# Optimization experiments

Hardware: AMD Instinct MI355X
Metric: run time of the kernel (lower is better)

The kernel has to match this reference:

```python
import jax, jax.numpy as jnp
import numpy as np

BS, NE, NN, CIN, H, D = 8, 4800, 4981, 3, 128, 6
EPG = 19200
NEDGE = BS * EPG
N = BS * NE

PARAM_NAMES = [
    'enc_cw1','enc_cb1','enc_cw2','enc_cb2','enc_cw3','enc_clng','enc_clnb',
    'enc_ew1','enc_eb1','enc_ew2','enc_eb2','enc_ew3','enc_elng','enc_elnb',
    'p_ew1','p_eb1','p_ew2','p_eb2','p_ew3','p_elng','p_elnb',
    'p_nw1','p_nb1','p_nw2','p_nb2','p_nw3','p_nlng','p_nlnb',
    'dec_uw1','dec_ub1','dec_uw2','dec_ub2','dec_uw3','dec_ulng','dec_ulnb',
    'dec_cw1','dec_cb1','dec_cw2','dec_cb2','dec_cw3']


def setup_inputs():
    key = jax.random.key(0)
    ks = iter(jax.random.split(key, 64))
    def nrm(shape, s=0.1):
        return jax.random.normal(next(ks), shape, jnp.float32) * s
    inp = {}
    inp['x'] = jax.random.normal(next(ks), (BS * NN, CIN), jnp.float32)
    inp['elem_conn'] = jax.random.randint(next(ks), (NE, 4), 0, NN)
    inp['edge_index'] = jax.random.randint(next(ks), (2, NEDGE), 0, N)
    inp['enc_cw1'] = nrm((CIN, 4, 1)); inp['enc_cb1'] = nrm((CIN, 1), 0.01)
    inp['enc_cw2'] = nrm((CIN, 1, 1)); inp['enc_cb2'] = nrm((CIN, 1), 0.01)
    inp['enc_cw3'] = nrm((CIN, 1, 1))
    inp['enc_clng'] = jnp.ones((CIN, 1)); inp['enc_clnb'] = jnp.zeros((CIN, 1))
    inp['enc_ew1'] = nrm((CIN, H)); inp['enc_eb1'] = nrm((H,), 0.01)
    inp['enc_ew2'] = nrm((H, H)); inp['enc_eb2'] = nrm((H,), 0.01)
    inp['enc_ew3'] = nrm((H, H))
    inp['enc_elng'] = jnp.ones((H,)); inp['enc_elnb'] = jnp.zeros((H,))
    inp['p_ew1'] = nrm((D, 2 * H, H)); inp['p_eb1'] = nrm((D, H), 0.01)
    inp['p_ew2'] = nrm((D, H, H)); inp['p_eb2'] = nrm((D, H), 0.01)
    inp['p_ew3'] = nrm((D, H, H))
    inp['p_elng'] = jnp.ones((D, H)); inp['p_elnb'] = jnp.zeros((D, H))
    inp['p_nw1'] = nrm((D, 2 * H, H)); inp['p_nb1'] = nrm((D, H), 0.01)
    inp['p_nw2'] = nrm((D, H, H)); inp['p_nb2'] = nrm((D, H), 0.01)
    inp['p_nw3'] = nrm((D, H, H))
    inp['p_nlng'] = jnp.ones((D, H)); inp['p_nlnb'] = jnp.zeros((D, H))
    inp['dec_uw1'] = nrm((H, 1, 4)); inp['dec_ub1'] = nrm((H, 4), 0.01)
    inp['dec_uw2'] = nrm((H, 4, 4)); inp['dec_ub2'] = nrm((H, 4), 0.01)
    inp['dec_uw3'] = nrm((H, 4, 4))
    inp['dec_ulng'] = jnp.ones((H, 4)); inp['dec_ulnb'] = jnp.zeros((H, 4))
    inp['dec_cw1'] = nrm((H, CIN)); inp['dec_cb1'] = nrm((CIN,), 0.01)
    inp['dec_cw2'] = nrm((CIN, CIN)); inp['dec_cb2'] = nrm((CIN,), 0.01)
    inp['dec_cw3'] = nrm((CIN, CIN))
    return inp


def lrelu(x):
    return jnp.where(x >= 0, x, 0.2 * x)


def ln(x, g, b, axis=-1):
    m = jnp.mean(x, axis=axis, keepdims=True)
    v = jnp.var(x, axis=axis, keepdims=True)
    return (x - m) / jnp.sqrt(v + 1e-5) * g + b


def mlp(x, w1, b1, w2, b2, w3):
    h = lrelu(x @ w1 + b1)
    h = lrelu(h @ w2 + b2)
    return h @ w3


def _forward(fl, elem_conn, edge_index):
    x = fl[0]
    P = dict(zip(PARAM_NAMES, fl[1:]))
    # ---- Encoder: MeshCNN gather (4 mesh nodes per element) + per-channel MLP 4->1 ----
    xg = x.reshape(BS, NN, CIN)[:, elem_conn]                  # (BS, NE, 4, CIN)
    h = lrelu(jnp.einsum('beic,cio->beoc', xg, P['enc_cw1']) + P['enc_cb1'].T[None, None])
    h = lrelu(jnp.einsum('beic,cio->beoc', h, P['enc_cw2']) + P['enc_cb2'].T[None, None])
    h = jnp.einsum('beic,cio->beoc', h, P['enc_cw3'])
    h = ln(h, P['enc_clng'].T[None, None], P['enc_clnb'].T[None, None], axis=2)  # LayerNorm(1)
    h = h[:, :, 0, :].reshape(N, CIN)
    h = ln(mlp(h, P['enc_ew1'], P['enc_eb1'], P['enc_ew2'], P['enc_eb2'], P['enc_ew3']),
           P['enc_elng'], P['enc_elnb'])                       # (N, H)
    # ---- Processor: D GraphNet blocks, edge MLP + scatter-add + node MLP ----
    src, dest = edge_index[0], edge_index[1]
    stacked = (P['p_ew1'], P['p_eb1'], P['p_ew2'], P['p_eb2'], P['p_ew3'], P['p_elng'], P['p_elnb'],
               P['p_nw1'], P['p_nb1'], P['p_nw2'], P['p_nb2'], P['p_nw3'], P['p_nlng'], P['p_nlnb'])
    def step(hc, p):
        ew1, eb1, ew2, eb2, ew3, eg, ebv, nw1, nb1, nw2, nb2, nw3, ng, nbv = p
        msg = jnp.concatenate([hc[dest], hc[src]], axis=-1)    # (NEDGE, 2H)
        m = ln(mlp(msg, ew1, eb1, ew2, eb2, ew3), eg, ebv)
        aggr = jax.ops.segment_sum(m, dest, num_segments=N)
        hn = ln(mlp(jnp.concatenate([hc, aggr], axis=-1), nw1, nb1, nw2, nb2, nw3), ng, nbv)
        return hn, None
    h, _ = jax.lax.scan(step, h, stacked)
    # ---- Decoder: per-channel upsample 1->4 then index_add back to mesh nodes ----
    u = h.reshape(BS, NE, H)[:, :, None, :]                    # (BS, NE, 1, H)
    u = lrelu(jnp.einsum('beic,cio->beoc', u, P['dec_uw1']) + P['dec_ub1'].T[None, None])
    u = lrelu(jnp.einsum('beic,cio->beoc', u, P['dec_uw2']) + P['dec_ub2'].T[None, None])
    u = jnp.einsum('beic,cio->beoc', u, P['dec_uw3'])
    u = ln(u, P['dec_ulng'].T[None, None], P['dec_ulnb'].T[None, None], axis=2)  # (BS, NE, 4, H)
    out = jnp.zeros((BS, NN, H), u.dtype).at[:, elem_conn.reshape(-1)].add(u.reshape(BS, NE * 4, H))
    out = out.reshape(BS * NN, H)
    o = lrelu(out @ P['dec_cw1'] + P['dec_cb1'])
    o = lrelu(o @ P['dec_cw2'] + P['dec_cb2'])
    return o @ P['dec_cw3']


def reference(x, elem_conn, edge_index,
              enc_cw1, enc_cb1, enc_cw2, enc_cb2, enc_cw3, enc_clng, enc_clnb,
              enc_ew1, enc_eb1, enc_ew2, enc_eb2, enc_ew3, enc_elng, enc_elnb,
              p_ew1, p_eb1, p_ew2, p_eb2, p_ew3, p_elng, p_elnb,
              p_nw1, p_nb1, p_nw2, p_nb2, p_nw3, p_nlng, p_nlnb,
              dec_uw1, dec_ub1, dec_uw2, dec_ub2, dec_uw3, dec_ulng, dec_ulnb,
              dec_cw1, dec_cb1, dec_cw2, dec_cb2, dec_cw3):
    fl = (x, enc_cw1, enc_cb1, enc_cw2, enc_cb2, enc_cw3, enc_clng, enc_clnb,
          enc_ew1, enc_eb1, enc_ew2, enc_eb2, enc_ew3, enc_elng, enc_elnb,
          p_ew1, p_eb1, p_ew2, p_eb2, p_ew3, p_elng, p_elnb,
          p_nw1, p_nb1, p_nw2, p_nb2, p_nw3, p_nlng, p_nlnb,
          dec_uw1, dec_ub1, dec_uw2, dec_ub2, dec_uw3, dec_ulng, dec_ulnb,
          dec_cw1, dec_cb1, dec_cw2, dec_cb2, dec_cw3)
    return _forward(fl, elem_conn, edge_index)
```

## Files before the change

kernel.cpp:

```cpp
#include <hip/hip_runtime.h>
#include <hip/hip_fp16.h>
#include <math.h>

#define BS    8
#define NE    4800
#define NN    4981
#define CIN   3
#define HD    128
#define DBLK  6
#define NEDGE 153600
#define NTOT  38400
#define NMESH (BS*NN)
#define NNP   5120
#define EM    128

#define UW1T  0
#define UB1T  512
#define UW2T  1024
#define UB2T  3072
#define UW3T  3584
#define ULNGT 5632
#define ULNBT 6144
#define DWT_N 6656

typedef _Float16 f16;
typedef _Float16 f16x8 __attribute__((ext_vector_type(8)));
typedef float f32x4 __attribute__((ext_vector_type(4)));

__device__ __forceinline__ float lrelu(float x) { return x >= 0.0f ? x : 0.2f * x; }

__global__ __launch_bounds__(128)
void enc_const_kernel(const float* __restrict__ clnb,
                      const float* __restrict__ ew1, const float* __restrict__ eb1,
                      const float* __restrict__ ew2, const float* __restrict__ eb2,
                      const float* __restrict__ ew3,
                      const float* __restrict__ g, const float* __restrict__ b,
                      float* __restrict__ hv0) {
    __shared__ float s1[HD], s2[HD], s3[HD];
    int j = threadIdx.x;
    float a = eb1[j];
    for (int c = 0; c < CIN; ++c) a += clnb[c] * ew1[c * HD + j];
    s1[j] = lrelu(a);
    __syncthreads();
    a = eb2[j];
    for (int k = 0; k < HD; ++k) a += s1[k] * ew2[k * HD + j];
    s2[j] = lrelu(a);
    __syncthreads();
    a = 0.0f;
    for (int k = 0; k < HD; ++k) a += s2[k] * ew3[k * HD + j];
    s3[j] = a;
    __syncthreads();
    float m = 0.0f;
    for (int k = 0; k < HD; ++k) m += s3[k];
    m *= (1.0f / HD);
    float v = 0.0f;
    for (int k = 0; k < HD; ++k) { float d = s3[k] - m; v += d * d; }
    v *= (1.0f / HD);
    float rs = 1.0f / sqrtf(v + 1e-5f);
    hv0[j] = (s3[j] - m) * rs * g[j] + b[j];
}

__global__ __launch_bounds__(128)
void msg0_kernel(const float* __restrict__ hv0,
                 const float* __restrict__ ew1, const float* __restrict__ eb1,
                 const float* __restrict__ ew2, const float* __restrict__ eb2,
                 const float* __restrict__ ew3,
                 const float* __restrict__ g, const float* __restrict__ b,
                 float* __restrict__ m0) {
    __shared__ float s1[HD], s2[HD], s3[HD];
    int j = threadIdx.x;
    float a = eb1[j];
    for (int k = 0; k < HD; ++k) a += hv0[k] * (ew1[k * HD + j] + ew1[(k + HD) * HD + j]);
    s1[j] = lrelu(a);
    __syncthreads();
    a = eb2[j];
    for (int k = 0; k < HD; ++k) a += s1[k] * ew2[k * HD + j];
    s2[j] = lrelu(a);
    __syncthreads();
    a = 0.0f;
    for (int k = 0; k < HD; ++k) a += s2[k] * ew3[k * HD + j];
    s3[j] = a;
    __syncthreads();
    float m = 0.0f;
    for (int k = 0; k < HD; ++k) m += s3[k];
    m *= (1.0f / HD);
    float v = 0.0f;
    for (int k = 0; k < HD; ++k) { float d = s3[k] - m; v += d * d; }
    v *= (1.0f / HD);
    float rs = 1.0f / sqrtf(v + 1e-5f);
    m0[j] = (s3[j] - m) * rs * g[j] + b[j];
}

__global__ __launch_bounds__(256)
void init_h16_kernel(f16* __restrict__ h, const float* __restrict__ hv0, int n8) {
    __shared__ f16 v[HD];
    if (threadIdx.x < HD) v[threadIdx.x] = (f16)hv0[threadIdx.x];
    __syncthreads();
    for (int i = blockIdx.x * blockDim.x + threadIdx.x; i < n8; i += gridDim.x * blockDim.x)
        ((uint4*)h)[i] = ((const uint4*)v)[i & 15];
}

__global__ __launch_bounds__(256)
void conv_weights_kernel(const float* __restrict__ ew1, const float* __restrict__ ew2,
                         const float* __restrict__ ew3,
                         const float* __restrict__ nw1, const float* __restrict__ nw2,
                         const float* __restrict__ nw3, f16* __restrict__ wbuf) {
    int b = blockIdx.x;
    int d = b >> 3, m = b & 7;
    const float* src;
    switch (m) {
        case 0: src = ew1 + (size_t)d * 2 * HD * HD; break;
        case 1: src = ew1 + (size_t)d * 2 * HD * HD + HD * HD; break;
        case 2: src = ew2 + (size_t)d * HD * HD; break;
        case 3: src = ew3 + (size_t)d * HD * HD; break;
        case 4: src = nw1 + (size_t)d * 2 * HD * HD; break;
        case 5: src = nw1 + (size_t)d * 2 * HD * HD + HD * HD; break;
        case 6: src = nw2 + (size_t)d * HD * HD; break;
        default: src = nw3 + (size_t)d * HD * HD; break;
    }
    f16* out = wbuf + (size_t)b * HD * HD;
    for (int idx = threadIdx.x; idx < HD * HD; idx += 256) {
        int n = idx >> 7, k = idx & 127;
        out[idx] = (f16)src[k * HD + n];
    }
}

__global__ __launch_bounds__(256)
void conv_dec_weights(const float* __restrict__ uw1, const float* __restrict__ ub1,
                      const float* __restrict__ uw2, const float* __restrict__ ub2,
                      const float* __restrict__ uw3, const float* __restrict__ ulng,
                      const float* __restrict__ ulnb, float* __restrict__ dwt) {
    int tid = threadIdx.x;
    for (int idx = tid; idx < 512; idx += 256) {
        int o = idx >> 7, c = idx & 127;
        dwt[UW1T + idx] = uw1[c * 4 + o];
        dwt[UB1T + idx] = ub1[c * 4 + o];
        dwt[UB2T + idx] = ub2[c * 4 + o];
        dwt[ULNGT + idx] = ulng[c * 4 + o];
        dwt[ULNBT + idx] = ulnb[c * 4 + o];
    }
    for (int idx = tid; idx < 2048; idx += 256) {
        int io = idx >> 7, c = idx & 127;
        dwt[UW2T + idx] = uw2[c * 16 + io];
        dwt[UW3T + idx] = uw3[c * 16 + io];
    }
}

__global__ __launch_bounds__(256)
void csr_hist(const int* __restrict__ key, int* __restrict__ deg, int n) {
    int e = blockIdx.x * 256 + threadIdx.x;
    if (e < n) atomicAdd(&deg[key[e]], 1);
}

__global__ __launch_bounds__(256)
void csr_scan1(const int* __restrict__ deg, int* __restrict__ rowptr,
               int* __restrict__ bsum) {
    __shared__ int s[256];
    int i = blockIdx.x * 256 + threadIdx.x;
    int v = deg[i];
    s[threadIdx.x] = v;
    __syncthreads();
    for (int off = 1; off < 256; off <<= 1) {
        int t = (threadIdx.x >= off) ? s[threadIdx.x - off] : 0;
        __syncthreads();
        s[threadIdx.x] += t;
        __syncthreads();
    }
    rowptr[i] = s[threadIdx.x] - v;
    if (threadIdx.x == 255) bsum[blockIdx.x] = s[255];
}

__global__ __launch_bounds__(256)
void csr_scan2(int* __restrict__ bsum, int nb) {
    __shared__ int s[256];
    int v = (threadIdx.x < nb) ? bsum[threadIdx.x] : 0;
    s[threadIdx.x] = v;
    __syncthreads();
    for (int off = 1; off < 256; off <<= 1) {
        int t = (threadIdx.x >= off) ? s[threadIdx.x - off] : 0;
        __syncthreads();
        s[threadIdx.x] += t;
        __syncthreads();
    }
    if (threadIdx.x < nb) bsum[threadIdx.x] = s[threadIdx.x] - v;
}

__global__ __launch_bounds__(256)
void csr_scan3(int* __restrict__ rowptr, const int* __restrict__ bsum) {
    int i = blockIdx.x * 256 + threadIdx.x;
    rowptr[i] += bsum[blockIdx.x];
}

__global__ __launch_bounds__(256)
void csr_scatter(const int* __restrict__ dest, const int* __restrict__ srcv,
                 const int* __restrict__ rowptr, int* __restrict__ cursor,
                 int* __restrict__ dsorted, int* __restrict__ ssorted) {
    int e = blockIdx.x * 256 + threadIdx.x;
    int d = dest[e];
    int pos = rowptr[d] + atomicAdd(&cursor[d], 1);
    dsorted[pos] = d;
    ssorted[pos] = srcv[e];
}

__global__ __launch_bounds__(256)
void mesh_scatter(const int* __restrict__ conn, const int* __restrict__ mrow,
                  int* __restrict__ mcur, int* __restrict__ mslot, int n) {
    int idx = blockIdx.x * 256 + threadIdx.x;
    if (idx < n) {
        int nd = conn[idx];
        int pos = mrow[nd] + atomicAdd(&mcur[nd], 1);
        mslot[pos] = idx;
    }
}

template <int NT>
__device__ __forceinline__ void stage_w(const f16* __restrict__ Wg, f16 (*Bt)[HD + 8],
                                        int tid) {
    #pragma unroll
    for (int t = 0; t < 2048 / NT; ++t) {
        int idx = tid + t * NT;
        int r = idx >> 4, c = (idx & 15) * 8;
        *(uint4*)(&Bt[r][c]) = *(const uint4*)(Wg + (size_t)r * HD + c);
    }
}

__device__ __forceinline__ void mfma_pass(const f16 (*A)[HD + 8], const f16 (*Bt)[HD + 8],
                                          int rt_base, int ct_base, int ln, int quad,
                                          f32x4 acc[2][4]) {
    #pragma unroll
    for (int ks = 0; ks < 4; ++ks) {
        int kb = ks * 32 + quad * 8;
        f16x8 a0 = *(const f16x8*)(&A[rt_base + ln][kb]);
        f16x8 a1 = *(const f16x8*)(&A[rt_base + 16 + ln][kb]);
        #pragma unroll
        for (int c = 0; c < 4; ++c) {
            f16x8 b = *(const f16x8*)(&Bt[ct_base + c * 16 + ln][kb]);
            acc[0][c] = __builtin_amdgcn_mfma_f32_16x16x32_f16(a0, b, acc[0][c], 0, 0, 0);
            acc[1][c] = __builtin_amdgcn_mfma_f32_16x16x32_f16(a1, b, acc[1][c], 0, 0, 0);
        }
    }
}

__global__ __launch_bounds__(512, 4)
void gn_edge(const f16* __restrict__ P1, const f16* __restrict__ P2,
             const int* __restrict__ dsorted, const int* __restrict__ ssorted,
             const f16* __restrict__ W2, const f16* __restrict__ W3,
             const float* __restrict__ b1, const float* __restrict__ b2,
             const float* __restrict__ g, const float* __restrict__ bln,
             f16* __restrict__ msg) {
    __shared__ __align__(16) f16 As[EM][HD + 8];
    __shared__ __align__(16) f16 Bt[HD][HD + 8];
    __shared__ float red[EM][2][2];
    __shared__ int dS[EM], sS[EM];

    const int tid = threadIdx.x;
    const int base = blockIdx.x * EM;
    const int wave = tid >> 6, lane = tid & 63;
    const int ln = lane & 15, quad = lane >> 4;
    const int rt_base = (wave >> 1) * 32;
    const int ct_base = (wave & 1) * 64;
    const int half = wave & 1;

    if (tid < EM) dS[tid] = dsorted[base + tid];
    else if (tid < 2 * EM) sS[tid - EM] = ssorted[base + tid - EM];
    __syncthreads();

    stage_w<512>(W2, Bt, tid);
    #pragma unroll
    for (int t = 0; t < 4; ++t) {
        int idx = tid + t * 512;
        int r = idx >> 4, c = (idx & 15) * 8;
        f16x8 p1 = *(const f16x8*)(P1 + (size_t)dS[r] * HD + c);
        f16x8 p2 = *(const f16x8*)(P2 + (size_t)sS[r] * HD + c);
        float4 ba = *(const float4*)(b1 + c);
        float4 bb = *(const float4*)(b1 + c + 4);
        f16x8 o;
        o[0] = (f16)lrelu((float)p1[0] + (float)p2[0] + ba.x);
        o[1] = (f16)lrelu((float)p1[1] + (float)p2[1] + ba.y);
        o[2] = (f16)lrelu((float)p1[2] + (float)p2[2] + ba.z);
        o[3] = (f16)lrelu((float)p1[3] + (float)p2[3] + ba.w);
        o[4] = (f16)lrelu((float)p1[4] + (float)p2[4] + bb.x);
        o[5] = (f16)lrelu((float)p1[5] + (float)p2[5] + bb.y);
        o[6] = (f16)lrelu((float)p1[6] + (float)p2[6] + bb.z);
        o[7] = (f16)lrelu((float)p1[7] + (float)p2[7] + bb.w);
        *(f16x8*)(&As[r][c]) = o;
    }
    __syncthreads();

    f32x4 acc[2][4];

    #pragma unroll
    for (int c = 0; c < 4; ++c) {
        float bj = b2[ct_base + c * 16 + ln];
        f32x4 bb = {bj, bj, bj, bj};
        acc[0][c] = bb; acc[1][c] = bb;
    }
    mfma_pass(As, Bt, rt_base, ct_base, ln, quad, acc);
    __syncthreads();
    stage_w<512>(W3, Bt, tid);
    #pragma unroll
    for (int i = 0; i < 2; ++i)
        #pragma unroll
        for (int c = 0; c < 4; ++c)
            #pragma unroll
            for (int r = 0; r < 4; ++r)
                As[rt_base + i * 16 + quad * 4 + r][ct_base + c * 16 + ln] =
                    (f16)lrelu(acc[i][c][r]);
    __syncthreads();

    #pragma unroll
    for (int c = 0; c < 4; ++c) { f32x4 z = {0,0,0,0}; acc[0][c] = z; acc[1][c] = z; }
    mfma_pass(As, Bt, rt_base, ct_base, ln, quad, acc);

    #pragma unroll
    for (int i = 0; i < 2; ++i)
        #pragma unroll
        for (int r = 0; r < 4; ++r) {
            float s = acc[i][0][r] + acc[i][1][r] + acc[i][2][r] + acc[i][3][r];
            float q = acc[i][0][r] * acc[i][0][r] + acc[i][1][r] * acc[i][1][r] +
                      acc[i][2][r] * acc[i][2][r] + acc[i][3][r] * acc[i][3][r];
            s += __shfl_xor(s, 1); q += __shfl_xor(q, 1);
            s += __shfl_xor(s, 2); q += __shfl_xor(q, 2);
            s += __shfl_xor(s, 4); q += __shfl_xor(q, 4);
            s += __shfl_xor(s, 8); q += __shfl_xor(q, 8);
            if (ln == 0) {
                int row = rt_base + i * 16 + quad * 4 + r;
                red[row][half][0] = s;
                red[row][half][1] = q;
            }
        }
    __syncthreads();

    float gv[4], bv[4];
    #pragma unroll
    for (int c = 0; c < 4; ++c) {
        int col = ct_base + c * 16 + ln;
        gv[c] = g[col]; bv[c] = bln[col];
    }
    #pragma unroll
    for (int i = 0; i < 2; ++i)
        #pragma unroll
        for (int r = 0; r < 4; ++r) {
            int row = rt_base + i * 16 + quad * 4 + r;
            float s = red[row][0][0] + red[row][1][0];
            float q = red[row][0][1] + red[row][1][1];
            float m = s * (1.0f / HD);
            float var = q * (1.0f / HD) - m * m;
            float rs = 1.0f / sqrtf(var + 1e-5f);
            #pragma unroll
            for (int c = 0; c < 4; ++c) {
                int col = ct_base + c * 16 + ln;
                float v = (acc[i][c][r] - m) * rs * gv[c] + bv[c];
                msg[(size_t)(base + row) * HD + col] = (f16)v;
            }
        }
}

template <int AGGR, bool PROD>
__global__ __launch_bounds__(256, 3)
void gn_node(f16* __restrict__ h16, const f16* __restrict__ msg,
             const int* __restrict__ rowptr, const int* __restrict__ deg,
             const float* __restrict__ m0,
             const f16* __restrict__ W1a, const f16* __restrict__ W1b,
             const f16* __restrict__ W2, const f16* __restrict__ W3,
             const float* __restrict__ b1, const float* __restrict__ b2,
             const float* __restrict__ g, const float* __restrict__ bln,
             const f16* __restrict__ nW1a, const f16* __restrict__ nW1b,
             f16* __restrict__ P1, f16* __restrict__ P2) {
    __shared__ __align__(16) f16 As[64][HD + 8];
    __shared__ __align__(16) f16 Bt[HD][HD + 8];
    __shared__ float red[64][2][2];
    int* rpS = (int*)&red[0][0][0];
    int* dgS = rpS + 64;

    const int tid = threadIdx.x;
    const int base = blockIdx.x * 64;
    const int wave = tid >> 6, lane = tid & 63;
    const int ln = lane & 15, quad = lane >> 4;
    const int rt_base = (wave >> 1) * 32;
    const int ct_base = (wave & 1) * 64;
    const int half = wave & 1;

    if (tid < 64) {
        if (AGGR == 1) rpS[tid] = rowptr[base + tid];
        dgS[tid] = deg[base + tid];
    }
    __syncthreads();

    f16x8 hreg[4];
    #pragma unroll
    for (int t = 0; t < 4; ++t) {
        int idx = tid + t * 256;
        int r = idx >> 4, c = (idx & 15) * 8;
        hreg[t] = *(const f16x8*)(h16 + (size_t)(base + r) * HD + c);
        if (AGGR == 0) {
            float sc = (float)dgS[r];
            f16x8 o;
            #pragma unroll
            for (int u = 0; u < 8; ++u) o[u] = (f16)(sc * m0[c + u]);
            *(f16x8*)(&As[r][c]) = o;
        } else {
            int rp = rpS[r], dg = dgS[r];
            float a[8] = {0, 0, 0, 0, 0, 0, 0, 0};
            for (int j = 0; j < dg; ++j) {
                f16x8 mv = *(const f16x8*)(msg + (size_t)(rp + j) * HD + c);
                #pragma unroll
                for (int u = 0; u < 8; ++u) a[u] += (float)mv[u];
            }
            f16x8 o;
            #pragma unroll
            for (int u = 0; u < 8; ++u) o[u] = (f16)a[u];
            *(f16x8*)(&As[r][c]) = o;
        }
    }
    stage_w<256>(W1b, Bt, tid);
    __syncthreads();

    f32x4 acc[2][4];
    #pragma unroll
    for (int c = 0; c < 4; ++c) {
        float bj = b1[ct_base + c * 16 + ln];
        f32x4 bb = {bj, bj, bj, bj};
        acc[0][c] = bb; acc[1][c] = bb;
    }
    mfma_pass(As, Bt, rt_base, ct_base, ln, quad, acc);
    __syncthreads();

    #pragma unroll
    for (int t = 0; t < 4; ++t) {
        int idx = tid + t * 256;
        int r = idx >> 4, c = (idx & 15) * 8;
        *(f16x8*)(&As[r][c]) = hreg[t];
    }
    stage_w<256>(W1a, Bt, tid);
    __syncthreads();
    mfma_pass(As, Bt, rt_base, ct_base, ln, quad, acc);
    __syncthreads();

    stage_w<256>(W2, Bt, tid);
    #pragma unroll
    for (int i = 0; i < 2; ++i)
        #pragma unroll
        for (int c = 0; c < 4; ++c)
            #pragma unroll
            for (int r = 0; r < 4; ++r)
                As[rt_base + i * 16 + quad * 4 + r][ct_base + c * 16 + ln] =
                    (f16)lrelu(acc[i][c][r]);
    __syncthreads();

    #pragma unroll
    for (int c = 0; c < 4; ++c) {
        float bj = b2[ct_base + c * 16 + ln];
        f32x4 bb = {bj, bj, bj, bj};
        acc[0][c] = bb; acc[1][c] = bb;
    }
    mfma_pass(As, Bt, rt_base, ct_base, ln, quad, acc);
    __syncthreads();
    stage_w<256>(W3, Bt, tid);
    #pragma unroll
    for (int i = 0; i < 2; ++i)
        #pragma unroll
        for (int c = 0; c < 4; ++c)
            #pragma unroll
            for (int r = 0; r < 4; ++r)
                As[rt_base + i * 16 + quad * 4 + r][ct_base + c * 16 + ln] =
                    (f16)lrelu(acc[i][c][r]);
    __syncthreads();

    #pragma unroll
    for (int c = 0; c < 4; ++c) { f32x4 z = {0,0,0,0}; acc[0][c] = z; acc[1][c] = z; }
    mfma_pass(As, Bt, rt_base, ct_base, ln, quad, acc);

    #pragma unroll
    for (int i = 0; i < 2; ++i)
        #pragma unroll
        for (int r = 0; r < 4; ++r) {
            float s = acc[i][0][r] + acc[i][1][r] + acc[i][2][r] + acc[i][3][r];
            float q = acc[i][0][r] * acc[i][0][r] + acc[i][1][r] * acc[i][1][r] +
                      acc[i][2][r] * acc[i][2][r] + acc[i][3][r] * acc[i][3][r];
            s += __shfl_xor(s, 1); q += __shfl_xor(q, 1);
            s += __shfl_xor(s, 2); q += __shfl_xor(q, 2);
            s += __shfl_xor(s, 4); q += __shfl_xor(q, 4);
            s += __shfl_xor(s, 8); q += __shfl_xor(q, 8);
            if (ln == 0) {
                int row = rt_base + i * 16 + quad * 4 + r;
                red[row][half][0] = s;
                red[row][half][1] = q;
            }
        }
    __syncthreads();

    float gv[4], bv[4];
    #pragma unroll
    for (int c = 0; c < 4; ++c) {
        int col = ct_base + c * 16 + ln;
        gv[c] = g[col]; bv[c] = bln[col];
    }
    #pragma unroll
    for (int i = 0; i < 2; ++i)
        #pragma unroll
        for (int r = 0; r < 4; ++r) {
            int row = rt_base + i * 16 + quad * 4 + r;
            float s = red[row][0][0] + red[row][1][0];
            float q = red[row][0][1] + red[row][1][1];
            float m = s * (1.0f / HD);
            float var = q * (1.0f / HD) - m * m;
            float rs = 1.0f / sqrtf(var + 1e-5f);
            #pragma unroll
            for (int c = 0; c < 4; ++c) {
                int col = ct_base + c * 16 + ln;
                float v = (acc[i][c][r] - m) * rs * gv[c] + bv[c];
                f16 hv = (f16)v;
                h16[(size_t)(base + row) * HD + col] = hv;
                if (PROD) As[row][col] = hv;
            }
        }

    if (PROD) {
        __syncthreads();
        stage_w<256>(nW1a, Bt, tid);
        __syncthreads();
        #pragma unroll
        for (int c = 0; c < 4; ++c) { f32x4 z = {0,0,0,0}; acc[0][c] = z; acc[1][c] = z; }
        mfma_pass(As, Bt, rt_base, ct_base, ln, quad, acc);
        #pragma unroll
        for (int i = 0; i < 2; ++i)
            #pragma unroll
            for (int c = 0; c < 4; ++c)
                #pragma unroll
                for (int r = 0; r < 4; ++r)
                    P1[(size_t)(base + rt_base + i * 16 + quad * 4 + r) * HD +
                       ct_base + c * 16 + ln] = (f16)acc[i][c][r];
        __syncthreads();
        stage_w<256>(nW1b, Bt, tid);
        __syncthreads();
        #pragma unroll
        for (int c = 0; c < 4; ++c) { f32x4 z = {0,0,0,0}; acc[0][c] = z; acc[1][c] = z; }
        mfma_pass(As, Bt, rt_base, ct_base, ln, quad, acc);
        #pragma unroll
        for (int i = 0; i < 2; ++i)
            #pragma unroll
            for (int c = 0; c < 4; ++c)
                #pragma unroll
                for (int r = 0; r < 4; ++r)
                    P2[(size_t)(base + rt_base + i * 16 + quad * 4 + r) * HD +
                       ct_base + c * 16 + ln] = (f16)acc[i][c][r];
    }
}

__global__ __launch_bounds__(256)
void dec_store_kernel(const f16* __restrict__ h, const float* __restrict__ dwt,
                      f16* __restrict__ uval) {
    __shared__ f16 ub[2][4][HD];
    int tid = threadIdx.x;
    int idx = blockIdx.x * 256 + tid;
    int c = idx & 127;
    int nl = tid >> 7;
    float s = (float)h[idx];
    float u1[4], u2[4], u3[4];
    #pragma unroll
    for (int o = 0; o < 4; ++o)
        u1[o] = lrelu(s * dwt[UW1T + o * 128 + c] + dwt[UB1T + o * 128 + c]);
    #pragma unroll
    for (int o = 0; o < 4; ++o) {
        float a = dwt[UB2T + o * 128 + c];
        #pragma unroll
        for (int i = 0; i < 4; ++i) a += u1[i] * dwt[UW2T + (i * 4 + o) * 128 + c];
        u2[o] = lrelu(a);
    }
    #pragma unroll
    for (int o = 0; o < 4; ++o) {
        float a = 0.f;
        #pragma unroll
        for (int i = 0; i < 4; ++i) a += u2[i] * dwt[UW3T + (i * 4 + o) * 128 + c];
        u3[o] = a;
    }
    float m = 0.25f * (u3[0] + u3[1] + u3[2] + u3[3]);
    float var = 0.f;
    #pragma unroll
    for (int o = 0; o < 4; ++o) { float d = u3[o] - m; var += d * d; }
    var *= 0.25f;
    float rs = 1.0f / sqrtf(var + 1e-5f);
    #pragma unroll
    for (int o = 0; o < 4; ++o) {
        float val = (u3[o] - m) * rs * dwt[ULNGT + o * 128 + c] + dwt[ULNBT + o * 128 + c];
        ub[nl][o][c] = (f16)val;
    }
    __syncthreads();
    int nl2 = tid >> 7, rem = tid & 127;
    uint2 v = ((const uint2*)&ub[nl2][0][0])[rem];
    ((uint2*)(uval + (size_t)(blockIdx.x * 2 + nl2) * 4 * HD))[rem] = v;
}

__global__ __launch_bounds__(256)
void dec_gather_out(const f16* __restrict__ uval,
                    const int* __restrict__ mrow, const int* __restrict__ mdeg,
                    const int* __restrict__ mslot,
                    const float* __restrict__ cw1, const float* __restrict__ cb1,
                    const float* __restrict__ cw2, const float* __restrict__ cb2,
                    const float* __restrict__ cw3,
                    float* __restrict__ o, int nrows) {
    int r = blockIdx.x * 4 + (threadIdx.x >> 6);
    if (r >= nrows) return;
    int lane = threadIdx.x & 63;
    int b = r / NN, n = r - b * NN;
    int rp = mrow[n], dg = mdeg[n];
    size_t boff = (size_t)b * NE * 4;
    float a0 = 0.f, a1 = 0.f;
    for (int j = 0; j < dg; ++j) {
        int slot = mslot[rp + j];
        const f16* up = uval + (boff + slot) * HD + lane * 2;
        a0 += (float)up[0];
        a1 += (float)up[1];
    }
    int c0 = lane * 2, c1 = lane * 2 + 1;
    float s[3];
    #pragma unroll
    for (int k = 0; k < 3; ++k)
        s[k] = a0 * cw1[c0 * 3 + k] + a1 * cw1[c1 * 3 + k];
    #pragma unroll
    for (int off = 32; off >= 1; off >>= 1) {
        s[0] += __shfl_down(s[0], off);
        s[1] += __shfl_down(s[1], off);
        s[2] += __shfl_down(s[2], off);
    }
    if (lane == 0) {
        float t1[3], t2[3];
        #pragma unroll
        for (int k = 0; k < 3; ++k) t1[k] = lrelu(s[k] + cb1[k]);
        #pragma unroll
        for (int k = 0; k < 3; ++k) {
            float a = cb2[k];
            #pragma unroll
            for (int q = 0; q < 3; ++q) a += t1[q] * cw2[q * 3 + k];
            t2[k] = lrelu(a);
        }
        #pragma unroll
        for (int k = 0; k < 3; ++k) {
            float a = 0.f;
            #pragma unroll
            for (int q = 0; q < 3; ++q) a += t2[q] * cw3[q * 3 + k];
            o[(size_t)r * 3 + k] = a;
        }
    }
}

extern "C" void kernel_launch(void* const* d_in, const int* in_sizes, int n_in,
                              void* d_out, int out_size, void* d_ws, size_t ws_size,
                              hipStream_t stream) {
    const int* elem_conn = (const int*)d_in[1];
    const int* edge_index = (const int*)d_in[2];
    const int* e_src = edge_index;
    const int* e_dst = edge_index + NEDGE;
    const float* enc_clnb = (const float*)d_in[9];
    const float* enc_ew1 = (const float*)d_in[10];
    const float* enc_eb1 = (const float*)d_in[11];
    const float* enc_ew2 = (const float*)d_in[12];
    const float* enc_eb2 = (const float*)d_in[13];
    const float* enc_ew3 = (const float*)d_in[14];
    const float* enc_elng = (const float*)d_in[15];
    const float* enc_elnb = (const float*)d_in[16];
    const float* p_ew1 = (const float*)d_in[17];
    const float* p_eb1 = (const float*)d_in[18];
    const float* p_ew2 = (const float*)d_in[19];
    const float* p_eb2 = (const float*)d_in[20];
    const float* p_ew3 = (const float*)d_in[21];
    const float* p_elng = (const float*)d_in[22];
    const float* p_elnb = (const float*)d_in[23];
    const float* p_nw1 = (const float*)d_in[24];
    const float* p_nb1 = (const float*)d_in[25];
    const float* p_nw2 = (const float*)d_in[26];
    const float* p_nb2 = (const float*)d_in[27];
    const float* p_nw3 = (const float*)d_in[28];
    const float* p_nlng = (const float*)d_in[29];
    const float* p_nlnb = (const float*)d_in[30];
    const float* dec_uw1 = (const float*)d_in[31];
    const float* dec_ub1 = (const float*)d_in[32];
    const float* dec_uw2 = (const float*)d_in[33];
    const float* dec_ub2 = (const float*)d_in[34];
    const float* dec_uw3 = (const float*)d_in[35];
    const float* dec_ulng = (const float*)d_in[36];
    const float* dec_ulnb = (const float*)d_in[37];
    const float* dec_cw1 = (const float*)d_in[38];
    const float* dec_cb1 = (const float*)d_in[39];
    const float* dec_cw2 = (const float*)d_in[40];
    const float* dec_cb2 = (const float*)d_in[41];
    const float* dec_cw3 = (const float*)d_in[42];

    char* ws = (char*)d_ws;
    f16*   h16     = (f16*)(ws);
    f16*   wbuf    = (f16*)(ws + 9830400);
    float* hv0     = (float*)(ws + 11403264);
    float* m0      = (float*)(ws + 11403776);
    f16*   P1      = (f16*)(ws + 11404288);
    f16*   P2      = (f16*)(ws + 21234688);
    f16*   msg     = (f16*)(ws + 31065088);
    f16*   uval    = (f16*)(ws + 31065088);
    int*   deg     = (int*)(ws + 70386688);
    int*   rowptr  = (int*)(ws + 70540288);
    int*   cursor  = (int*)(ws + 70693888);
    int*   bsum    = (int*)(ws + 70847488);
    int*   dsorted = (int*)(ws + 70848512);
    int*   ssorted = (int*)(ws + 71462912);
    int*   mdeg    = (int*)(ws + 70693888);
    int*   mrow    = (int*)(ws + 70714368);
    int*   mcur    = (int*)(ws + 70734848);
    int*   mbsum   = (int*)(ws + 70755328);
    int*   mslot   = (int*)(ws + 70756352);
    float* dwt     = (float*)P1;

    enc_const_kernel<<<1, 128, 0, stream>>>(enc_clnb, enc_ew1, enc_eb1, enc_ew2,
                                            enc_eb2, enc_ew3, enc_elng, enc_elnb, hv0);
    init_h16_kernel<<<1200, 256, 0, stream>>>(h16, hv0, NTOT * HD / 8);
    conv_weights_kernel<<<48, 256, 0, stream>>>(p_ew1, p_ew2, p_ew3,
                                                p_nw1, p_nw2, p_nw3, wbuf);
    msg0_kernel<<<1, 128, 0, stream>>>(hv0, p_ew1, p_eb1, p_ew2, p_eb2, p_ew3,
                                       p_elng, p_elnb, m0);

    hipMemsetAsync(deg, 0, NTOT * sizeof(int), stream);
    hipMemsetAsync(cursor, 0, NTOT * sizeof(int), stream);
    csr_hist<<<NEDGE / 256, 256, 0, stream>>>(e_dst, deg, NEDGE);
    csr_scan1<<<NTOT / 256, 256, 0, stream>>>(deg, rowptr, bsum);
    csr_scan2<<<1, 256, 0, stream>>>(bsum, NTOT / 256);
    csr_scan3<<<NTOT / 256, 256, 0, stream>>>(rowptr, bsum);
    csr_scatter<<<NEDGE / 256, 256, 0, stream>>>(e_dst, e_src, rowptr, cursor,
                                                 dsorted, ssorted);

    hipMemsetAsync(mdeg, 0, NNP * sizeof(int), stream);
    hipMemsetAsync(mcur, 0, NNP * sizeof(int), stream);
    csr_hist<<<(NE * 4 + 255) / 256, 256, 0, stream>>>(elem_conn, mdeg, NE * 4);
    csr_scan1<<<NNP / 256, 256, 0, stream>>>(mdeg, mrow, mbsum);
    csr_scan2<<<1, 256, 0, stream>>>(mbsum, NNP / 256);
    csr_scan3<<<NNP / 256, 256, 0, stream>>>(mrow, mbsum);
    mesh_scatter<<<(NE * 4 + 255) / 256, 256, 0, stream>>>(elem_conn, mrow, mcur,
                                                           mslot, NE * 4);

    {
        const f16* wd = wbuf;
        const f16* wn = wbuf + (size_t)8 * HD * HD;
        gn_node<0, true><<<NTOT / 64, 256, 0, stream>>>(
            h16, nullptr, nullptr, deg, m0,
            wd + 4 * HD * HD, wd + 5 * HD * HD, wd + 6 * HD * HD, wd + 7 * HD * HD,
            p_nb1, p_nb2, p_nlng, p_nlnb,
            wn + 0 * HD * HD, wn + 1 * HD * HD, P1, P2);
    }

    for (int d = 1; d < DBLK; ++d) {
        const f16* wd = wbuf + (size_t)d * 8 * HD * HD;
        gn_edge<<<NEDGE / EM, 512, 0, stream>>>(
            P1, P2, dsorted, ssorted,
            wd + 2 * HD * HD, wd + 3 * HD * HD,
            p_eb1 + (size_t)d * HD, p_eb2 + (size_t)d * HD,
            p_elng + (size_t)d * HD, p_elnb + (size_t)d * HD, msg);
        if (d < DBLK - 1) {
            const f16* wn = wbuf + (size_t)(d + 1) * 8 * HD * HD;
            gn_node<1, true><<<NTOT / 64, 256, 0, stream>>>(
                h16, msg, rowptr, deg, nullptr,
                wd + 4 * HD * HD, wd + 5 * HD * HD, wd + 6 * HD * HD, wd + 7 * HD * HD,
                p_nb1 + (size_t)d * HD, p_nb2 + (size_t)d * HD,
                p_nlng + (size_t)d * HD, p_nlnb + (size_t)d * HD,
                wn + 0 * HD * HD, wn + 1 * HD * HD, P1, P2);
        } else {
            gn_node<1, false><<<NTOT / 64, 256, 0, stream>>>(
                h16, msg, rowptr, deg, nullptr,
                wd + 4 * HD * HD, wd + 5 * HD * HD, wd + 6 * HD * HD, wd + 7 * HD * HD,
                p_nb1 + (size_t)d * HD, p_nb2 + (size_t)d * HD,
                p_nlng + (size_t)d * HD, p_nlnb + (size_t)d * HD,
                wbuf, wbuf, P1, P2);
        }
    }

    conv_dec_weights<<<1, 256, 0, stream>>>(dec_uw1, dec_ub1, dec_uw2, dec_ub2,
                                            dec_uw3, dec_ulng, dec_ulnb, dwt);
    dec_store_kernel<<<NTOT * HD / 256, 256, 0, stream>>>(h16, dwt, uval);
    dec_gather_out<<<(NMESH + 3) / 4, 256, 0, stream>>>(
        uval, mrow, mdeg, mslot, dec_cw1, dec_cb1, dec_cw2, dec_cb2, dec_cw3,
        (float*)d_out, NMESH);
}
```

Before: 642.6 us.

## Halve edge-kernel weight LDS tile to raise occupancy, stage K in two halves

The edge MLP kernel now stages each 128x128 weight matrix into shared memory in two 64-wide K halves, shrinking the B tile from 128x136 to 128x72 halves. The LayerNorm reduction buffer is aliased onto that tile, and launch bounds are raised from 4 to 6 blocks per CU. The goal is to cut LDS per block so more blocks can be resident and gather latency is better hidden. In exchange it adds extra __syncthreads and staging phases per block, and the tighter launch bound may force register spills.

New measurement: 663.9 us. +3.3%, slower.

```diff
diff --git a/kernel.cpp b/kernel.cpp
--- a/kernel.cpp
+++ b/kernel.cpp
@@ -241,7 +241,35 @@
     }
 }
 
-__global__ __launch_bounds__(512, 4)
+__device__ __forceinline__ void stage_w_half(const f16* __restrict__ Wg,
+                                             f16 (*Bt)[64 + 8], int tid, int kh) {
+    #pragma unroll
+    for (int t = 0; t < 2; ++t) {
+        int idx = tid + t * 512;
+        int r = idx >> 3, c = (idx & 7) * 8;
+        *(uint4*)(&Bt[r][c]) = *(const uint4*)(Wg + (size_t)r * HD + kh * 64 + c);
+    }
+}
+
+__device__ __forceinline__ void mfma_pass_half(const f16 (*A)[HD + 8],
+                                               const f16 (*Bt)[64 + 8],
+                                               int rt_base, int ct_base, int ln, int quad,
+                                               int koff, f32x4 acc[2][4]) {
+    #pragma unroll
+    for (int ks = 0; ks < 2; ++ks) {
+        int kb = ks * 32 + quad * 8;
+        f16x8 a0 = *(const f16x8*)(&A[rt_base + ln][koff + kb]);
+        f16x8 a1 = *(const f16x8*)(&A[rt_base + 16 + ln][koff + kb]);
+        #pragma unroll
+        for (int c = 0; c < 4; ++c) {
+            f16x8 b = *(const f16x8*)(&Bt[ct_base + c * 16 + ln][kb]);
+            acc[0][c] = __builtin_amdgcn_mfma_f32_16x16x32_f16(a0, b, acc[0][c], 0, 0, 0);
+            acc[1][c] = __builtin_amdgcn_mfma_f32_16x16x32_f16(a1, b, acc[1][c], 0, 0, 0);
+        }
+    }
+}
+
+__global__ __launch_bounds__(512, 6)
 void gn_edge(const f16* __restrict__ P1, const f16* __restrict__ P2,
              const int* __restrict__ dsorted, const int* __restrict__ ssorted,
              const f16* __restrict__ W2, const f16* __restrict__ W3,
@@ -249,9 +277,9 @@
              const float* __restrict__ g, const float* __restrict__ bln,
              f16* __restrict__ msg) {
     __shared__ __align__(16) f16 As[EM][HD + 8];
-    __shared__ __align__(16) f16 Bt[HD][HD + 8];
-    __shared__ float red[EM][2][2];
+    __shared__ __align__(16) f16 Bt[EM][64 + 8];
     __shared__ int dS[EM], sS[EM];
+    float (*red)[2][2] = (float(*)[2][2])&Bt[0][0];
 
     const int tid = threadIdx.x;
     const int base = blockIdx.x * EM;
@@ -265,7 +293,7 @@
     else if (tid < 2 * EM) sS[tid - EM] = ssorted[base + tid - EM];
     __syncthreads();
 
-    stage_w<512>(W2, Bt, tid);
+    stage_w_half(W2, Bt, tid, 0);
     #pragma unroll
     for (int t = 0; t < 4; ++t) {
         int idx = tid + t * 512;
@@ -295,9 +323,14 @@
         f32x4 bb = {bj, bj, bj, bj};
         acc[0][c] = bb; acc[1][c] = bb;
     }
-    mfma_pass(As, Bt, rt_base, ct_base, ln, quad, acc);
-    __syncthreads();
-    stage_w<512>(W3, Bt, tid);
+    mfma_pass_half(As, Bt, rt_base, ct_base, ln, quad, 0, acc);
+    __syncthreads();
+    stage_w_half(W2, Bt, tid, 1);
+    __syncthreads();
+    mfma_pass_half(As, Bt, rt_base, ct_base, ln, quad, 64, acc);
+    __syncthreads();
+
+    stage_w_half(W3, Bt, tid, 0);
     #pragma unroll
     for (int i = 0; i < 2; ++i)
         #pragma unroll
@@ -310,7 +343,12 @@
 
     #pragma unroll
     for (int c = 0; c < 4; ++c) { f32x4 z = {0,0,0,0}; acc[0][c] = z; acc[1][c] = z; }
-    mfma_pass(As, Bt, rt_base, ct_base, ln, quad, acc);
+    mfma_pass_half(As, Bt, rt_base, ct_base, ln, quad, 0, acc);
+    __syncthreads();
+    stage_w_half(W3, Bt, tid, 1);
+    __syncthreads();
+    mfma_pass_half(As, Bt, rt_base, ct_base, ln, quad, 64, acc);
+    __syncthreads();
 
     #pragma unroll
     for (int i = 0; i < 2; ++i)
```
